# Optimization experiments

Hardware: AMD Instinct MI355X
Metric: run time of the kernel (lower is better)

Reference implementation:

```python
import jax, jax.numpy as jnp
import numpy as np

E = 1024
H = 16
F = 4096
EPS = 1e-5


def layer_norm(x, gamma, beta):
    mu = jnp.mean(x, axis=-1, keepdims=True)
    var = jnp.var(x, axis=-1, keepdims=True)
    return (x - mu) * jax.lax.rsqrt(var + EPS) * gamma + beta


def setup_inputs() -> dict:
    key = jax.random.key(0)
    ks = jax.random.split(key, 12)
    s = lambda d: 1.0 / np.sqrt(d)
    x = jax.random.normal(ks[0], (2, 2048, E), dtype=jnp.float32)
    Wq = jax.random.uniform(ks[1], (E, E), minval=-s(E), maxval=s(E))
    bq = jnp.zeros((E,), jnp.float32)
    Wk = jax.random.uniform(ks[2], (E, E), minval=-s(E), maxval=s(E))
    bk = jnp.zeros((E,), jnp.float32)
    Wv = jax.random.uniform(ks[3], (E, E), minval=-s(E), maxval=s(E))
    bv = jnp.zeros((E,), jnp.float32)
    Wo = jax.random.uniform(ks[4], (E, E), minval=-s(E), maxval=s(E))
    bo = jnp.zeros((E,), jnp.float32)
    g1 = jnp.ones((E,), jnp.float32)
    b1 = jnp.zeros((E,), jnp.float32)
    W1 = jax.random.uniform(ks[5], (E, F), minval=-s(E), maxval=s(E))
    bf1 = jnp.zeros((F,), jnp.float32)
    W2 = jax.random.uniform(ks[6], (F, E), minval=-s(F), maxval=s(F))
    bf2 = jnp.zeros((E,), jnp.float32)
    g2 = jnp.ones((E,), jnp.float32)
    b2 = jnp.zeros((E,), jnp.float32)
    return dict(x=x, Wq=Wq, bq=bq, Wk=Wk, bk=bk, Wv=Wv, bv=bv, Wo=Wo, bo=bo,
                g1=g1, b1=b1, W1=W1, bf1=bf1, W2=W2, bf2=bf2, g2=g2, b2=b2)


def reference(x, Wq, bq, Wk, bk, Wv, bv, Wo, bo, g1, b1, W1, bf1, W2, bf2, g2, b2):
    B, L, _ = x.shape
    Dh = E // H
    q = (x @ Wq + bq).reshape(B, L, H, Dh).transpose(0, 2, 1, 3)  # b h l d
    k = (x @ Wk + bk).reshape(B, L, H, Dh).transpose(0, 2, 1, 3)  # computed but unused (faithful to source)
    v = (x @ Wv + bv).reshape(B, L, H, Dh).transpose(0, 2, 1, 3)
    # NOTE: source computes scores as Q @ V^T (not K), scaled, then softmax
    scores = jnp.einsum('bhqd,bhkd->bhqk', q, v) / jnp.sqrt(jnp.float32(Dh))
    att = jax.nn.softmax(scores, axis=-1)
    ctx = jnp.einsum('bhqk,bhkd->bhqd', att, v)
    ctx = ctx.transpose(0, 2, 1, 3).reshape(B, L, E)
    att_out = ctx @ Wo + bo
    post_att = layer_norm(x + att_out, g1, b1)
    ff = jax.nn.relu(post_att @ W1 + bf1) @ W2 + bf2
    return layer_norm(post_att + ff, g2, b2)
```

## Files before the change

### kernel.cpp

```cpp
#include <hip/hip_runtime.h>
#include <stdint.h>

typedef unsigned short u16;
typedef __attribute__((ext_vector_type(8))) short short8;
typedef __attribute__((ext_vector_type(4))) float f32x4;
typedef __attribute__((ext_vector_type(4))) unsigned short u16x4;

#define TOKENS 4096
#define E_DIM 1024
#define F_DIM 4096
#define SEQ 2048
#define NH 16
#define DH 64

__device__ __forceinline__ u16 f2b(float f) {
  union { float f; unsigned u; } v; v.f = f;
  unsigned r = v.u + 0x7fffu + ((v.u >> 16) & 1u);
  return (u16)(r >> 16);
}

__device__ __forceinline__ void gl2lds16(const u16* g, u16* l) {
  __builtin_amdgcn_global_load_lds(
      (const __attribute__((address_space(1))) unsigned int*)(size_t)(g),
      (__attribute__((address_space(3))) unsigned int*)(unsigned int)(size_t)(l),
      16, 0, 0);
}

__global__ __launch_bounds__(256)
void transpose_w(const float* __restrict__ W, u16* __restrict__ Wt, int K, int N) {
  __shared__ float tile[32][33];
  const int kb = blockIdx.x * 32, nb = blockIdx.y * 32;
  const int tx = threadIdx.x & 31, ty = threadIdx.x >> 5;
#pragma unroll
  for (int i = 0; i < 32; i += 8)
    tile[ty + i][tx] = W[(size_t)(kb + ty + i) * N + nb + tx];
  __syncthreads();
#pragma unroll
  for (int i = 0; i < 32; i += 8)
    Wt[(size_t)(nb + ty + i) * K + kb + tx] = f2b(tile[tx][ty + i]);
}

__global__ __launch_bounds__(256)
void f32_to_bf16(const float* __restrict__ in, u16* __restrict__ out) {
  const int i = blockIdx.x * 256 + threadIdx.x;
  f32x4 f = ((const f32x4*)in)[i];
  u16x4 u;
#pragma unroll
  for (int j = 0; j < 4; j++) u[j] = f2b(f[j]);
  ((u16x4*)out)[i] = u;
}

__global__ __launch_bounds__(256)
void transpose_v(const u16* __restrict__ vsrc, u16* __restrict__ vt) {
  __shared__ u16 tile[64][66];
  const int kb = blockIdx.x * 64;
  const int bh = blockIdx.y;
  const int b = bh >> 4, h = bh & 15;
  {
    const int d = threadIdx.x & 63, r = threadIdx.x >> 6;
#pragma unroll
    for (int i = 0; i < 64; i += 4)
      tile[r + i][d] = vsrc[(size_t)(b * SEQ + kb + r + i) * E_DIM + h * DH + d];
  }
  __syncthreads();
  {
    const int pos = threadIdx.x & 63;
    const int srck = (pos & 3) * 16 + (pos >> 2);
#pragma unroll
    for (int j = 0; j < 64; j += 4) {
      const int d = (threadIdx.x >> 6) + j;
      vt[(size_t)(bh * DH + d) * SEQ + kb + pos] = tile[srck][d];
    }
  }
}

template <int RELU, int OUTBF>
__global__ __launch_bounds__(256)
void gemm_bt(const u16* __restrict__ A, const u16* __restrict__ Bt,
             const float* __restrict__ bias, void* __restrict__ Cout,
             int M, int N, int K) {
  __shared__ __align__(16) u16 As[128 * 32];
  __shared__ __align__(16) u16 Bs[128 * 32];
  const int tid = threadIdx.x;
  const int lane = tid & 63, wave = tid >> 6;
  const int mBlk = blockIdx.y * 128, nBlk = blockIdx.x * 128;
  const int wm = (wave >> 1) * 64, wn = (wave & 1) * 64;
  const int l15 = lane & 15, g = lane >> 4;

  f32x4 acc[4][4] = {};
  const int srow = lane >> 2;
  const int scol = (lane & 3) * 8;

  const u16* Ab = A + (size_t)mBlk * K;
  const u16* Bb = Bt + (size_t)nBlk * K;

  for (int k0 = 0; k0 < K; k0 += 32) {
    __syncthreads();
    for (int c = wave; c < 8; c += 4) {
      const int r = c * 16 + srow;
      gl2lds16(Ab + (size_t)r * K + k0 + scol, As + c * 512 + lane * 8);
      gl2lds16(Bb + (size_t)r * K + k0 + scol, Bs + c * 512 + lane * 8);
    }
    __syncthreads();

    short8 af[4], bf[4];
#pragma unroll
    for (int i = 0; i < 4; i++)
      af[i] = *(const short8*)(As + (wm + i * 16 + l15) * 32 + g * 8);
#pragma unroll
    for (int i = 0; i < 4; i++)
      bf[i] = *(const short8*)(Bs + (wn + i * 16 + l15) * 32 + g * 8);
#pragma unroll
    for (int mi = 0; mi < 4; mi++)
#pragma unroll
      for (int ni = 0; ni < 4; ni++)
        acc[mi][ni] = __builtin_amdgcn_mfma_f32_16x16x32_bf16(af[mi], bf[ni],
                                                              acc[mi][ni], 0, 0, 0);
  }

  const int row0 = mBlk + wm + g * 4;
  const int col0 = nBlk + wn + l15;
#pragma unroll
  for (int ni = 0; ni < 4; ni++) {
    const int c = col0 + ni * 16;
    const float bv = bias[c];
#pragma unroll
    for (int mi = 0; mi < 4; mi++) {
#pragma unroll
      for (int r = 0; r < 4; r++) {
        float v = acc[mi][ni][r] + bv;
        if (RELU) v = fmaxf(v, 0.f);
        const size_t idx = (size_t)(row0 + mi * 16 + r) * N + c;
        if (OUTBF) ((u16*)Cout)[idx] = f2b(v);
        else       ((float*)Cout)[idx] = v;
      }
    }
  }
}

template <int RELU, int OUTBF>
__global__ __launch_bounds__(512)
void gemm256(const u16* __restrict__ A, const u16* __restrict__ Bt,
             const float* __restrict__ bias, void* __restrict__ Cout,
             int N, int K) {
  __shared__ __align__(16) u16 lds[3][2][8192];
  const int tid = threadIdx.x;
  const int lane = tid & 63, wave = tid >> 6;
  const int wm = wave >> 2, wn = wave & 3;
  const int l15 = lane & 15, g = lane >> 4;

  const int bid = blockIdx.x;
  const int xcd = bid & 7, idx = bid >> 3;
  const int mT = (xcd >> 2) * 8 + (idx >> 2);
  const int nT = (xcd & 3) * 4 + (idx & 3);
  const int mBlk = mT * 256, nBlk = nT * 256;

  const u16* Ab = A + (size_t)mBlk * K;
  const u16* Bb = Bt + (size_t)nBlk * K;

  const int sm = lane >> 2;
  const int sk = (lane & 3) * 8;
  const u16* sa0 = Ab + (size_t)(wave * 16 + sm) * K + sk;
  const u16* sa1 = Ab + (size_t)((8 + wave) * 16 + sm) * K + sk;
  const u16* sb0 = Bb + (size_t)(wave * 16 + sm) * K + sk;
  const u16* sb1 = Bb + (size_t)((8 + wave) * 16 + sm) * K + sk;

  f32x4 acc[8][4] = {};

  const int NT = K >> 5;

#define STAGE_A(buf, t)                                             \
  {                                                                 \
    gl2lds16(sa0 + (size_t)(t) * 32, &lds[buf][0][wave * 512 + lane * 8]);       \
    gl2lds16(sa1 + (size_t)(t) * 32, &lds[buf][0][(8 + wave) * 512 + lane * 8]); \
  }
#define STAGE_B(buf, t)                                             \
  {                                                                 \
    gl2lds16(sb0 + (size_t)(t) * 32, &lds[buf][1][wave * 512 + lane * 8]);       \
    gl2lds16(sb1 + (size_t)(t) * 32, &lds[buf][1][(8 + wave) * 512 + lane * 8]); \
  }

  STAGE_A(0, 0) STAGE_B(0, 0)
  STAGE_A(1, 1) STAGE_B(1, 1)
  asm volatile("s_waitcnt vmcnt(4)" ::: "memory");
  asm volatile("s_barrier" ::: "memory");

  int buf = 0, sbuf = 2;
  for (int t = 0; t < NT; ++t) {
    const u16* As_ = &lds[buf][0][wm * (8 * 512)];
    const u16* Bs_ = &lds[buf][1][wn * (4 * 512)];
    const int fo = l15 * 32 + g * 8;

    short8 af[4], bfr[4];
#pragma unroll
    for (int i = 0; i < 4; i++)
      af[i] = *(const short8*)(As_ + i * 512 + fo);
#pragma unroll
    for (int i = 0; i < 4; i++)
      bfr[i] = *(const short8*)(Bs_ + i * 512 + fo);
    if (t + 2 < NT) STAGE_A(sbuf, t + 2)
    asm volatile("s_barrier" ::: "memory");
    asm volatile("s_waitcnt lgkmcnt(0)" ::: "memory");
    __builtin_amdgcn_sched_barrier(0);
    __builtin_amdgcn_s_setprio(1);
#pragma unroll
    for (int mg = 0; mg < 4; mg++)
#pragma unroll
      for (int ng = 0; ng < 4; ng++)
        acc[mg][ng] = __builtin_amdgcn_mfma_f32_16x16x32_bf16(af[mg], bfr[ng],
                                                              acc[mg][ng], 0, 0, 0);
    __builtin_amdgcn_s_setprio(0);
    asm volatile("s_barrier" ::: "memory");

#pragma unroll
    for (int i = 0; i < 4; i++)
      af[i] = *(const short8*)(As_ + (4 + i) * 512 + fo);
    if (t + 2 < NT) STAGE_B(sbuf, t + 2)
    asm volatile("s_barrier" ::: "memory");
    asm volatile("s_waitcnt lgkmcnt(0)" ::: "memory");
    __builtin_amdgcn_sched_barrier(0);
    __builtin_amdgcn_s_setprio(1);
#pragma unroll
    for (int mg = 0; mg < 4; mg++)
#pragma unroll
      for (int ng = 0; ng < 4; ng++)
        acc[4 + mg][ng] = __builtin_amdgcn_mfma_f32_16x16x32_bf16(af[mg], bfr[ng],
                                                                  acc[4 + mg][ng], 0, 0, 0);
    __builtin_amdgcn_s_setprio(0);
    if (t + 2 < NT) asm volatile("s_waitcnt vmcnt(4)" ::: "memory");
    else            asm volatile("s_waitcnt vmcnt(0)" ::: "memory");
    asm volatile("s_barrier" ::: "memory");

    buf = (buf == 2) ? 0 : buf + 1;
    sbuf = (sbuf == 2) ? 0 : sbuf + 1;
  }
#undef STAGE_A
#undef STAGE_B

  const int row0 = mBlk + wm * 128 + g * 4;
  const int col0 = nBlk + wn * 64 + l15;
#pragma unroll
  for (int ng = 0; ng < 4; ng++) {
    const int c = col0 + ng * 16;
    const float bv = bias[c];
#pragma unroll
    for (int mg = 0; mg < 8; mg++) {
#pragma unroll
      for (int r = 0; r < 4; r++) {
        float v = acc[mg][ng][r] + bv;
        if (RELU) v = fmaxf(v, 0.f);
        const size_t o = (size_t)(row0 + mg * 16 + r) * N + c;
        if (OUTBF) ((u16*)Cout)[o] = f2b(v);
        else       ((float*)Cout)[o] = v;
      }
    }
  }
}

__global__ __launch_bounds__(256)
void gemm_bt_sk(const u16* __restrict__ A, const u16* __restrict__ Bt,
                const float* __restrict__ bias, float* __restrict__ Cout,
                int M, int N, int K) {
  __shared__ __align__(16) u16 As[128 * 32];
  __shared__ __align__(16) u16 Bs[128 * 32];
  const int tid = threadIdx.x;
  const int lane = tid & 63, wave = tid >> 6;
  const int mBlk = blockIdx.y * 128, nBlk = blockIdx.x * 128;
  const int kz = blockIdx.z;
  const int Kh = K >> 1;
  const int wm = (wave >> 1) * 64, wn = (wave & 1) * 64;
  const int l15 = lane & 15, g = lane >> 4;

  f32x4 acc[4][4] = {};
  const int srow = lane >> 2;
  const int scol = (lane & 3) * 8;

  const u16* Ab = A + (size_t)mBlk * K + (size_t)kz * Kh;
  const u16* Bb = Bt + (size_t)nBlk * K + (size_t)kz * Kh;

  for (int k0 = 0; k0 < Kh; k0 += 32) {
    __syncthreads();
    for (int c = wave; c < 8; c += 4) {
      const int r = c * 16 + srow;
      gl2lds16(Ab + (size_t)r * K + k0 + scol, As + c * 512 + lane * 8);
      gl2lds16(Bb + (size_t)r * K + k0 + scol, Bs + c * 512 + lane * 8);
    }
    __syncthreads();

    short8 af[4], bf[4];
#pragma unroll
    for (int i = 0; i < 4; i++)
      af[i] = *(const short8*)(As + (wm + i * 16 + l15) * 32 + g * 8);
#pragma unroll
    for (int i = 0; i < 4; i++)
      bf[i] = *(const short8*)(Bs + (wn + i * 16 + l15) * 32 + g * 8);
#pragma unroll
    for (int mi = 0; mi < 4; mi++)
#pragma unroll
      for (int ni = 0; ni < 4; ni++)
        acc[mi][ni] = __builtin_amdgcn_mfma_f32_16x16x32_bf16(af[mi], bf[ni],
                                                              acc[mi][ni], 0, 0, 0);
  }

  float* out = Cout + (size_t)kz * M * N;
  const int row0 = mBlk + wm + g * 4;
  const int col0 = nBlk + wn + l15;
#pragma unroll
  for (int ni = 0; ni < 4; ni++) {
    const int c = col0 + ni * 16;
    const float bv = (kz == 0) ? bias[c] : 0.f;
#pragma unroll
    for (int mi = 0; mi < 4; mi++) {
#pragma unroll
      for (int r = 0; r < 4; r++)
        out[(size_t)(row0 + mi * 16 + r) * N + c] = acc[mi][ni][r] + bv;
    }
  }
}

__global__ __launch_bounds__(256)
void gemm_qv64(const u16* __restrict__ A, const u16* __restrict__ Bqv,
               const float* __restrict__ bq, const float* __restrict__ bv,
               u16* __restrict__ qout, u16* __restrict__ vout, int K) {
  __shared__ __align__(16) u16 As[128 * 32];
  __shared__ __align__(16) u16 Bs[64 * 32];
  const int tid = threadIdx.x;
  const int lane = tid & 63, wave = tid >> 6;
  const int mBlk = blockIdx.y * 128, nBlk = blockIdx.x * 64;
  const int isQ = nBlk < 1024;
  const int ncol = isQ ? nBlk : nBlk - 1024;
  const float* bias = isQ ? bq : bv;
  u16* out = isQ ? qout : vout;
  const float oscale = isQ ? 0.125f : 1.0f;
  const int wm = (wave >> 1) * 64, wn = (wave & 1) * 32;
  const int l15 = lane & 15, g = lane >> 4;

  f32x4 acc[4][2] = {};
  const int srow = lane >> 2;
  const int scol = (lane & 3) * 8;

  const u16* Ab = A + (size_t)mBlk * K;
  const u16* Bb = Bqv + (size_t)nBlk * K;

  for (int k0 = 0; k0 < K; k0 += 32) {
    __syncthreads();
    for (int c = wave; c < 8; c += 4) {
      const int r = c * 16 + srow;
      gl2lds16(Ab + (size_t)r * K + k0 + scol, As + c * 512 + lane * 8);
    }
    gl2lds16(Bb + (size_t)(wave * 16 + srow) * K + k0 + scol, Bs + wave * 512 + lane * 8);
    __syncthreads();

    short8 af[4], bf[2];
#pragma unroll
    for (int i = 0; i < 4; i++)
      af[i] = *(const short8*)(As + (wm + i * 16 + l15) * 32 + g * 8);
#pragma unroll
    for (int i = 0; i < 2; i++)
      bf[i] = *(const short8*)(Bs + (wn + i * 16 + l15) * 32 + g * 8);
#pragma unroll
    for (int mi = 0; mi < 4; mi++)
#pragma unroll
      for (int ni = 0; ni < 2; ni++)
        acc[mi][ni] = __builtin_amdgcn_mfma_f32_16x16x32_bf16(af[mi], bf[ni],
                                                              acc[mi][ni], 0, 0, 0);
  }

  const int row0 = mBlk + wm + g * 4;
  const int col0 = ncol + wn + l15;
#pragma unroll
  for (int ni = 0; ni < 2; ni++) {
    const int c = col0 + ni * 16;
    const float bv_ = bias[c];
#pragma unroll
    for (int mi = 0; mi < 4; mi++) {
#pragma unroll
      for (int r = 0; r < 4; r++) {
        float v = (acc[mi][ni][r] + bv_) * oscale;
        out[(size_t)(row0 + mi * 16 + r) * E_DIM + c] = f2b(v);
      }
    }
  }
}

__global__ __launch_bounds__(128)
void attn_kernel(const u16* __restrict__ qb, const u16* __restrict__ vb,
                 const u16* __restrict__ vtb, u16* __restrict__ ctxb) {
  __shared__ __align__(16) u16 Vs[2][64 * 64];
  __shared__ __align__(16) u16 Vts[2][64 * 64];
  __shared__ __align__(16) u16 Pl[2][32 * 64];
  const int tid = threadIdx.x;
  const int lane = tid & 63;
  const int wave = tid >> 6;
  const int l15 = lane & 15;
  const int g = lane >> 4;
  const int qblk = blockIdx.x;
  const int bh = blockIdx.y;
  const int b = bh >> 4;
  const int h = bh & 15;
  const int qrow = qblk * 64 + wave * 32;

  short8 aq[2][2];
#pragma unroll
  for (int sub = 0; sub < 2; sub++) {
    const u16* qp = qb + ((size_t)(b * SEQ + qrow + sub * 16 + l15)) * E_DIM + h * DH + g * 8;
    aq[sub][0] = *(const short8*)(qp);
    aq[sub][1] = *(const short8*)(qp + 32);
  }

  f32x4 o[2][4] = {};
  float lsum[2][4] = {};

  const u16* vbase = vb + ((size_t)b * SEQ) * E_DIM + h * DH;
  const u16* vtbase = vtb + ((size_t)bh * DH) * SEQ;
  u16* myPl = Pl[wave];

  const int srow = tid >> 3;
  const int sch = tid & 7;

#define STAGE(buf, kcv)                                                          \
  {                                                                              \
    const int kc_ = (kcv);                                                       \
    _Pragma("unroll") for (int j = 0; j < 4; j++) {                              \
      const int key = j * 16 + srow;                                             \
      gl2lds16(vbase + (size_t)(kc_ + key) * E_DIM + ((sch ^ (key & 7)) * 8),    \
               Vs[buf] + key * 64 + sch * 8);                                    \
      const int d = j * 16 + srow;                                               \
      gl2lds16(vtbase + (size_t)d * SEQ + kc_ + ((sch ^ (d & 7)) * 8),           \
               Vts[buf] + d * 64 + sch * 8);                                     \
    }                                                                            \
  }

  STAGE(0, 0)
  int cur = 0;

  for (int kc = 0; kc < SEQ; kc += 64) {
    asm volatile("s_barrier" ::: "memory");
    if (kc + 64 < SEQ) {
      STAGE(cur ^ 1, kc + 64)
      asm volatile("s_waitcnt vmcnt(8)" ::: "memory");
    } else {
      asm volatile("s_waitcnt vmcnt(0)" ::: "memory");
    }
    asm volatile("s_barrier" ::: "memory");

    const u16* VsC = Vs[cur];
    const u16* VtsC = Vts[cur];

    f32x4 s[2][4];
#pragma unroll
    for (int nt = 0; nt < 4; nt++) {
      const int key = nt * 16 + l15;
      const u16* vr = VsC + key * 64;
      short8 b0 = *(const short8*)(vr + ((g ^ (key & 7)) * 8));
      short8 b1 = *(const short8*)(vr + (((4 + g) ^ (key & 7)) * 8));
      f32x4 z0 = {}, z1 = {};
      z0 = __builtin_amdgcn_mfma_f32_16x16x32_bf16(aq[0][0], b0, z0, 0, 0, 0);
      z0 = __builtin_amdgcn_mfma_f32_16x16x32_bf16(aq[0][1], b1, z0, 0, 0, 0);
      z1 = __builtin_amdgcn_mfma_f32_16x16x32_bf16(aq[1][0], b0, z1, 0, 0, 0);
      z1 = __builtin_amdgcn_mfma_f32_16x16x32_bf16(aq[1][1], b1, z1, 0, 0, 0);
      s[0][nt] = z0;
      s[1][nt] = z1;
    }

#pragma unroll
    for (int sub = 0; sub < 2; sub++) {
#pragma unroll
      for (int r = 0; r < 4; r++) {
        const int row = sub * 16 + g * 4 + r;
        union { float f; unsigned u; } p0, p1, p2, p3;
        p0.f = __expf(s[sub][0][r]);
        p1.f = __expf(s[sub][1][r]);
        p2.f = __expf(s[sub][2][r]);
        p3.f = __expf(s[sub][3][r]);
        union { unsigned u; float f; } t0, t1, t2, t3;
        t0.u = p0.u & 0xffff0000u;
        t1.u = p1.u & 0xffff0000u;
        t2.u = p2.u & 0xffff0000u;
        t3.u = p3.u & 0xffff0000u;
        lsum[sub][r] += (t0.f + t1.f) + (t2.f + t3.f);
        uint2 pk;
        pk.x = __builtin_amdgcn_perm(p1.u, p0.u, 0x07060302u);
        pk.y = __builtin_amdgcn_perm(p3.u, p2.u, 0x07060302u);
        *(uint2*)(myPl + row * 64 + (((l15 >> 1) ^ (row & 7)) << 3) + ((l15 & 1) << 2)) = pk;
      }
    }

#pragma unroll
    for (int ks = 0; ks < 2; ks++) {
      const int row0_ = l15, row1_ = 16 + l15;
      short8 ap0 = *(const short8*)(myPl + row0_ * 64 + (((ks * 4 + g) ^ (row0_ & 7)) << 3));
      short8 ap1 = *(const short8*)(myPl + row1_ * 64 + (((ks * 4 + g) ^ (row1_ & 7)) << 3));
#pragma unroll
      for (int dt = 0; dt < 4; dt++) {
        const int d = dt * 16 + l15;
        short8 bv = *(const short8*)(VtsC + d * 64 + (((ks * 4 + g) ^ (d & 7)) * 8));
        o[0][dt] = __builtin_amdgcn_mfma_f32_16x16x32_bf16(ap0, bv, o[0][dt], 0, 0, 0);
        o[1][dt] = __builtin_amdgcn_mfma_f32_16x16x32_bf16(ap1, bv, o[1][dt], 0, 0, 0);
      }
    }
    cur ^= 1;
  }
#undef STAGE

#pragma unroll
  for (int sub = 0; sub < 2; sub++) {
#pragma unroll
    for (int r = 0; r < 4; r++) {
      float l = lsum[sub][r];
      l += __shfl_xor(l, 1);
      l += __shfl_xor(l, 2);
      l += __shfl_xor(l, 4);
      l += __shfl_xor(l, 8);
      const float inv = 1.0f / l;
      size_t base = ((size_t)(b * SEQ + qrow + sub * 16 + g * 4 + r)) * E_DIM + h * DH;
#pragma unroll
      for (int dt = 0; dt < 4; dt++)
        ctxb[base + dt * 16 + l15] = f2b(o[sub][dt][r] * inv);
    }
  }
}

__global__ __launch_bounds__(256)
void add_ln3(const float* __restrict__ X, const float* __restrict__ Y0,
             const float* __restrict__ Y1,
             const float* __restrict__ gam, const float* __restrict__ bet,
             float* __restrict__ out32, u16* __restrict__ out16) {
  const int row = blockIdx.x;
  const int tid = threadIdx.x;
  const size_t base = (size_t)row * E_DIM;
  float v[4];
  float s = 0.f, sq = 0.f;
#pragma unroll
  for (int i = 0; i < 4; i++) {
    const int c = tid + i * 256;
    float x = X[base + c] + Y0[base + c] + Y1[base + c];
    v[i] = x; s += x; sq += x * x;
  }
#pragma unroll
  for (int off = 32; off; off >>= 1) {
    s += __shfl_xor(s, off);
    sq += __shfl_xor(sq, off);
  }
  __shared__ float sh[8];
  const int wave = tid >> 6, lane = tid & 63;
  if (lane == 0) { sh[wave] = s; sh[4 + wave] = sq; }
  __syncthreads();
  s = sh[0] + sh[1] + sh[2] + sh[3];
  sq = sh[4] + sh[5] + sh[6] + sh[7];
  const float mean = s * (1.f / 1024.f);
  const float var = sq * (1.f / 1024.f) - mean * mean;
  const float rstd = rsqrtf(var + 1e-5f);
#pragma unroll
  for (int i = 0; i < 4; i++) {
    const int c = tid + i * 256;
    float y = (v[i] - mean) * rstd * gam[c] + bet[c];
    out32[base + c] = y;
    if (out16) out16[base + c] = f2b(y);
  }
}

extern "C" void kernel_launch(void* const* d_in, const int* in_sizes, int n_in,
                              void* d_out, int out_size, void* d_ws, size_t ws_size,
                              hipStream_t stream) {
  const float* x   = (const float*)d_in[0];
  const float* Wq  = (const float*)d_in[1];
  const float* bq  = (const float*)d_in[2];
  const float* Wv  = (const float*)d_in[5];
  const float* bv  = (const float*)d_in[6];
  const float* Wo  = (const float*)d_in[7];
  const float* bo  = (const float*)d_in[8];
  const float* g1  = (const float*)d_in[9];
  const float* b1  = (const float*)d_in[10];
  const float* W1  = (const float*)d_in[11];
  const float* bf1 = (const float*)d_in[12];
  const float* W2  = (const float*)d_in[13];
  const float* bf2 = (const float*)d_in[14];
  const float* g2  = (const float*)d_in[15];
  const float* b2  = (const float*)d_in[16];

  char* w = (char*)d_ws;
  const size_t MB = 1024ull * 1024ull;
  u16*   xb   = (u16*)(w + 0);
  u16*   h1   = (u16*)(w + 8 * MB);
  u16*   qb   = (u16*)(w + 8 * MB);
  u16*   vb   = (u16*)(w + 16 * MB);
  u16*   vtb  = (u16*)(w + 24 * MB);
  u16*   ctxb = (u16*)(w + 32 * MB);
  float* att0 = (float*)(w + 40 * MB);
  float* ff0  = (float*)(w + 40 * MB);
  float* pa   = (float*)(w + 72 * MB);
  u16*   pab  = (u16*)(w + 88 * MB);
  u16*   WqT  = (u16*)(w + 96 * MB);
  u16*   WvT  = (u16*)(w + 98 * MB);
  u16*   WoT  = (u16*)(w + 100 * MB);
  u16*   W1T  = (u16*)(w + 102 * MB);
  u16*   W2T  = (u16*)(w + 110 * MB);

  transpose_w<<<dim3(32, 32), 256, 0, stream>>>(Wq, WqT, 1024, 1024);
  transpose_w<<<dim3(32, 32), 256, 0, stream>>>(Wv, WvT, 1024, 1024);
  transpose_w<<<dim3(32, 32), 256, 0, stream>>>(Wo, WoT, 1024, 1024);
  transpose_w<<<dim3(32, 128), 256, 0, stream>>>(W1, W1T, 1024, 4096);
  transpose_w<<<dim3(128, 32), 256, 0, stream>>>(W2, W2T, 4096, 1024);
  f32_to_bf16<<<TOKENS * E_DIM / 4 / 256, 256, 0, stream>>>(x, xb);

  gemm_qv64<<<dim3(32, 32), 256, 0, stream>>>(xb, WqT, bq, bv, qb, vb, 1024);
  transpose_v<<<dim3(32, 32), 256, 0, stream>>>(vb, vtb);
  attn_kernel<<<dim3(32, 32), 128, 0, stream>>>(qb, vb, vtb, ctxb);
  gemm_bt_sk<<<dim3(8, 32, 2), 256, 0, stream>>>(ctxb, WoT, bo, att0, TOKENS, 1024, 1024);
  add_ln3<<<TOKENS, 256, 0, stream>>>(x, att0, att0 + (size_t)TOKENS * 1024, g1, b1, pa, pab);
  gemm256<1, 1><<<dim3(256), 512, 0, stream>>>(pab, W1T, bf1, h1, 4096, 1024);
  gemm_bt_sk<<<dim3(8, 32, 2), 256, 0, stream>>>(h1, W2T, bf2, ff0, TOKENS, 1024, 4096);
  add_ln3<<<TOKENS, 256, 0, stream>>>(pa, ff0, ff0 + (size_t)TOKENS * 1024, g2, b2, (float*)d_out, (u16*)nullptr);
}
```

Before: 381.2 us.

## Split attention block into four waves of 16 query rows, fold log2e into Q

The attention kernel now runs 256 threads (4 waves) per 64-query block, each wave owning 16 query rows instead of 32. Staging of the V and V-transposed tiles is spread over more threads with precomputed, incremented pointers, so each thread issues fewer loads. The Q projection pre-multiplies by log2(e), which lets the softmax use the hardware exp2 directly instead of __expf. The aim is more waves to hide latency and cheaper address math, at the cost of each wave reusing every loaded V fragment across fewer MFMAs.

```diff
diff --git a/kernel.cpp b/kernel.cpp
--- a/kernel.cpp
+++ b/kernel.cpp
@@ -331,7 +331,7 @@
   const int ncol = isQ ? nBlk : nBlk - 1024;
   const float* bias = isQ ? bq : bv;
   u16* out = isQ ? qout : vout;
-  const float oscale = isQ ? 0.125f : 1.0f;
+  const float oscale = isQ ? 0.125f * 1.44269504088896f : 1.0f;
   const int wm = (wave >> 1) * 64, wn = (wave & 1) * 32;
   const int l15 = lane & 15, g = lane >> 4;
 
@@ -383,12 +383,12 @@
   }
 }
 
-__global__ __launch_bounds__(128)
+__global__ __launch_bounds__(256)
 void attn_kernel(const u16* __restrict__ qb, const u16* __restrict__ vb,
                  const u16* __restrict__ vtb, u16* __restrict__ ctxb) {
   __shared__ __align__(16) u16 Vs[2][64 * 64];
   __shared__ __align__(16) u16 Vts[2][64 * 64];
-  __shared__ __align__(16) u16 Pl[2][32 * 64];
+  __shared__ __align__(16) u16 Pl[4][16 * 64];
   const int tid = threadIdx.x;
   const int lane = tid & 63;
   const int wave = tid >> 6;
@@ -398,47 +398,46 @@
   const int bh = blockIdx.y;
   const int b = bh >> 4;
   const int h = bh & 15;
-  const int qrow = qblk * 64 + wave * 32;
-
-  short8 aq[2][2];
-#pragma unroll
-  for (int sub = 0; sub < 2; sub++) {
-    const u16* qp = qb + ((size_t)(b * SEQ + qrow + sub * 16 + l15)) * E_DIM + h * DH + g * 8;
-    aq[sub][0] = *(const short8*)(qp);
-    aq[sub][1] = *(const short8*)(qp + 32);
-  }
-
-  f32x4 o[2][4] = {};
-  float lsum[2][4] = {};
-
-  const u16* vbase = vb + ((size_t)b * SEQ) * E_DIM + h * DH;
-  const u16* vtbase = vtb + ((size_t)bh * DH) * SEQ;
+  const int qrow = qblk * 64 + wave * 16;
+
+  short8 aq0, aq1;
+  {
+    const u16* qp = qb + ((size_t)(b * SEQ + qrow + l15)) * E_DIM + h * DH + g * 8;
+    aq0 = *(const short8*)(qp);
+    aq1 = *(const short8*)(qp + 32);
+  }
+
+  f32x4 o[4] = {};
+  float lsum[4] = {};
+
   u16* myPl = Pl[wave];
 
   const int srow = tid >> 3;
   const int sch = tid & 7;
-
-#define STAGE(buf, kcv)                                                          \
-  {                                                                              \
-    const int kc_ = (kcv);                                                       \
-    _Pragma("unroll") for (int j = 0; j < 4; j++) {                              \
-      const int key = j * 16 + srow;                                             \
-      gl2lds16(vbase + (size_t)(kc_ + key) * E_DIM + ((sch ^ (key & 7)) * 8),    \
-               Vs[buf] + key * 64 + sch * 8);                                    \
-      const int d = j * 16 + srow;                                               \
-      gl2lds16(vtbase + (size_t)d * SEQ + kc_ + ((sch ^ (d & 7)) * 8),           \
-               Vts[buf] + d * 64 + sch * 8);                                     \
-    }                                                                            \
-  }
-
-  STAGE(0, 0)
+  const int r0 = srow, r1 = 32 + srow;
+  const u16* pv0 = vb + ((size_t)(b * SEQ) + r0) * E_DIM + h * DH + ((sch ^ (r0 & 7)) * 8);
+  const u16* pv1 = vb + ((size_t)(b * SEQ) + r1) * E_DIM + h * DH + ((sch ^ (r1 & 7)) * 8);
+  const u16* pt0 = vtb + ((size_t)bh * DH + r0) * SEQ + ((sch ^ (r0 & 7)) * 8);
+  const u16* pt1 = vtb + ((size_t)bh * DH + r1) * SEQ + ((sch ^ (r1 & 7)) * 8);
+
+#define STAGE(buf)                                      \
+  {                                                     \
+    gl2lds16(pv0, Vs[buf] + tid * 8);                   \
+    gl2lds16(pv1, Vs[buf] + 2048 + tid * 8);            \
+    gl2lds16(pt0, Vts[buf] + tid * 8);                  \
+    gl2lds16(pt1, Vts[buf] + 2048 + tid * 8);           \
+    pv0 += 64 * E_DIM; pv1 += 64 * E_DIM;               \
+    pt0 += 64; pt1 += 64;                               \
+  }
+
+  STAGE(0)
   int cur = 0;
 
   for (int kc = 0; kc < SEQ; kc += 64) {
     asm volatile("s_barrier" ::: "memory");
     if (kc + 64 < SEQ) {
-      STAGE(cur ^ 1, kc + 64)
-      asm volatile("s_waitcnt vmcnt(8)" ::: "memory");
+      STAGE(cur ^ 1)
+      asm volatile("s_waitcnt vmcnt(4)" ::: "memory");
     } else {
       asm volatile("s_waitcnt vmcnt(0)" ::: "memory");
     }
@@ -447,56 +446,48 @@
     const u16* VsC = Vs[cur];
     const u16* VtsC = Vts[cur];
 
-    f32x4 s[2][4];
+    f32x4 s[4];
 #pragma unroll
     for (int nt = 0; nt < 4; nt++) {
       const int key = nt * 16 + l15;
       const u16* vr = VsC + key * 64;
       short8 b0 = *(const short8*)(vr + ((g ^ (key & 7)) * 8));
       short8 b1 = *(const short8*)(vr + (((4 + g) ^ (key & 7)) * 8));
-      f32x4 z0 = {}, z1 = {};
-      z0 = __builtin_amdgcn_mfma_f32_16x16x32_bf16(aq[0][0], b0, z0, 0, 0, 0);
-      z0 = __builtin_amdgcn_mfma_f32_16x16x32_bf16(aq[0][1], b1, z0, 0, 0, 0);
-      z1 = __builtin_amdgcn_mfma_f32_16x16x32_bf16(aq[1][0], b0, z1, 0, 0, 0);
-      z1 = __builtin_amdgcn_mfma_f32_16x16x32_bf16(aq[1][1], b1, z1, 0, 0, 0);
-      s[0][nt] = z0;
-      s[1][nt] = z1;
-    }
-
-#pragma unroll
-    for (int sub = 0; sub < 2; sub++) {
-#pragma unroll
-      for (int r = 0; r < 4; r++) {
-        const int row = sub * 16 + g * 4 + r;
-        union { float f; unsigned u; } p0, p1, p2, p3;
-        p0.f = __expf(s[sub][0][r]);
-        p1.f = __expf(s[sub][1][r]);
-        p2.f = __expf(s[sub][2][r]);
-        p3.f = __expf(s[sub][3][r]);
-        union { unsigned u; float f; } t0, t1, t2, t3;
-        t0.u = p0.u & 0xffff0000u;
-        t1.u = p1.u & 0xffff0000u;
-        t2.u = p2.u & 0xffff0000u;
-        t3.u = p3.u & 0xffff0000u;
-        lsum[sub][r] += (t0.f + t1.f) + (t2.f + t3.f);
-        uint2 pk;
-        pk.x = __builtin_amdgcn_perm(p1.u, p0.u, 0x07060302u);
-        pk.y = __builtin_amdgcn_perm(p3.u, p2.u, 0x07060302u);
-        *(uint2*)(myPl + row * 64 + (((l15 >> 1) ^ (row & 7)) << 3) + ((l15 & 1) << 2)) = pk;
-      }
+      f32x4 z = {};
+      z = __builtin_amdgcn_mfma_f32_16x16x32_bf16(aq0, b0, z, 0, 0, 0);
+      z = __builtin_amdgcn_mfma_f32_16x16x32_bf16(aq1, b1, z, 0, 0, 0);
+      s[nt] = z;
+    }
+
+#pragma unroll
+    for (int r = 0; r < 4; r++) {
+      const int row = g * 4 + r;
+      union { float f; unsigned u; } p0, p1, p2, p3;
+      p0.f = __builtin_amdgcn_exp2f(s[0][r]);
+      p1.f = __builtin_amdgcn_exp2f(s[1][r]);
+      p2.f = __builtin_amdgcn_exp2f(s[2][r]);
+      p3.f = __builtin_amdgcn_exp2f(s[3][r]);
+      union { unsigned u; float f; } t0, t1, t2, t3;
+      t0.u = p0.u & 0xffff0000u;
+      t1.u = p1.u & 0xffff0000u;
+      t2.u = p2.u & 0xffff0000u;
+      t3.u = p3.u & 0xffff0000u;
+      lsum[r] += (t0.f + t1.f) + (t2.f + t3.f);
+      uint2 pk;
+      pk.x = __builtin_amdgcn_perm(p1.u, p0.u, 0x07060302u);
+      pk.y = __builtin_amdgcn_perm(p3.u, p2.u, 0x07060302u);
+      *(uint2*)(myPl + row * 64 + (((l15 >> 1) ^ (row & 7)) << 3) + ((l15 & 1) << 2)) = pk;
     }
 
 #pragma unroll
     for (int ks = 0; ks < 2; ks++) {
-      const int row0_ = l15, row1_ = 16 + l15;
-      short8 ap0 = *(const short8*)(myPl + row0_ * 64 + (((ks * 4 + g) ^ (row0_ & 7)) << 3));
-      short8 ap1 = *(const short8*)(myPl + row1_ * 64 + (((ks * 4 + g) ^ (row1_ & 7)) << 3));
+      const int rp = l15;
+      short8 ap = *(const short8*)(myPl + rp * 64 + (((ks * 4 + g) ^ (rp & 7)) << 3));
 #pragma unroll
       for (int dt = 0; dt < 4; dt++) {
         const int d = dt * 16 + l15;
         short8 bv = *(const short8*)(VtsC + d * 64 + (((ks * 4 + g) ^ (d & 7)) * 8));
-        o[0][dt] = __builtin_amdgcn_mfma_f32_16x16x32_bf16(ap0, bv, o[0][dt], 0, 0, 0);
-        o[1][dt] = __builtin_amdgcn_mfma_f32_16x16x32_bf16(ap1, bv, o[1][dt], 0, 0, 0);
+        o[dt] = __builtin_amdgcn_mfma_f32_16x16x32_bf16(ap, bv, o[dt], 0, 0, 0);
       }
     }
     cur ^= 1;
@@ -504,20 +495,17 @@
 #undef STAGE
 
 #pragma unroll
-  for (int sub = 0; sub < 2; sub++) {
-#pragma unroll
-    for (int r = 0; r < 4; r++) {
-      float l = lsum[sub][r];
-      l += __shfl_xor(l, 1);
-      l += __shfl_xor(l, 2);
-      l += __shfl_xor(l, 4);
-      l += __shfl_xor(l, 8);
-      const float inv = 1.0f / l;
-      size_t base = ((size_t)(b * SEQ + qrow + sub * 16 + g * 4 + r)) * E_DIM + h * DH;
-#pragma unroll
-      for (int dt = 0; dt < 4; dt++)
-        ctxb[base + dt * 16 + l15] = f2b(o[sub][dt][r] * inv);
-    }
+  for (int r = 0; r < 4; r++) {
+    float l = lsum[r];
+    l += __shfl_xor(l, 1);
+    l += __shfl_xor(l, 2);
+    l += __shfl_xor(l, 4);
+    l += __shfl_xor(l, 8);
+    const float inv = 1.0f / l;
+    size_t base = ((size_t)(b * SEQ + qrow + g * 4 + r)) * E_DIM + h * DH;
+#pragma unroll
+    for (int dt = 0; dt < 4; dt++)
+      ctxb[base + dt * 16 + l15] = f2b(o[dt][r] * inv);
   }
 }
 
@@ -606,7 +594,7 @@
 
   gemm_qv64<<<dim3(32, 32), 256, 0, stream>>>(xb, WqT, bq, bv, qb, vb, 1024);
   transpose_v<<<dim3(32, 32), 256, 0, stream>>>(vb, vtb);
-  attn_kernel<<<dim3(32, 32), 128, 0, stream>>>(qb, vb, vtb, ctxb);
+  attn_kernel<<<dim3(32, 32), 256, 0, stream>>>(qb, vb, vtb, ctxb);
   gemm_bt_sk<<<dim3(8, 32, 2), 256, 0, stream>>>(ctxb, WoT, bo, att0, TOKENS, 1024, 1024);
   add_ln3<<<TOKENS, 256, 0, stream>>>(x, att0, att0 + (size_t)TOKENS * 1024, g1, b1, pa, pab);
   gemm256<1, 1><<<dim3(256), 512, 0, stream>>>(pab, W1T, bf1, h1, 4096, 1024);
```

Measured after the change: 380.4 us. No clear change (-0.2%).
